# Kernel optimization log

Hardware: AMD Instinct MI355X
Metric: run time of the kernel (lower is better)

The kernel has to match this reference:

```python
import jax, jax.numpy as jnp
import numpy as np

RES_DIM = 8192
BATCH = 128
DENSITY = 0.02
NNZ = int(DENSITY * RES_DIM * RES_DIM)  # 1342177
LEAK = 0.6
BIAS = 1.6


def setup_inputs() -> dict:
    key = jax.random.key(0)
    k1, k2, k3, k4, k5 = jax.random.split(key, 5)
    proj_vars = jax.random.normal(k1, (BATCH, RES_DIM), dtype=jnp.float32)
    res_state = jax.random.normal(k2, (BATCH, RES_DIM), dtype=jnp.float32)
    # COO representation of the sparse reservoir matrix wr (what BCOO stores).
    # Values scaled so the effective spectral radius is O(spec_rad), keeping
    # tanh out of full saturation (init-time normalization detail).
    scale = 0.8 / np.sqrt(DENSITY * RES_DIM)
    wr_vals = jax.random.normal(k3, (NNZ,), dtype=jnp.float32) * scale
    wr_rows = jnp.sort(jax.random.randint(k4, (NNZ,), 0, RES_DIM, dtype=jnp.int32))
    wr_cols = jax.random.randint(k5, (NNZ,), 0, RES_DIM, dtype=jnp.int32)
    return {
        "proj_vars": proj_vars,
        "res_state": res_state,
        "wr_vals": wr_vals,
        "wr_rows": wr_rows,
        "wr_cols": wr_cols,
    }


def reference(proj_vars, res_state, wr_vals, wr_rows, wr_cols):
    # Batched sparse matvec: y[b, i] = sum_k vals[k] * res_state[b, cols[k]] for rows[k]==i
    # gather -> [nnz, batch], scale by vals, scatter-add over rows (sorted).
    contrib = wr_vals[:, None] * res_state.T[wr_cols]           # [nnz, B]
    y = jax.ops.segment_sum(contrib, wr_rows, num_segments=RES_DIM,
                            indices_are_sorted=True)            # [res_dim, B]
    res_next = jnp.tanh(y.T + proj_vars + BIAS)                  # [B, res_dim]
    return LEAK * res_next + (1.0 - LEAK) * res_state
```

## Files before the change

kernel.cpp:

```cpp
#include <hip/hip_runtime.h>
#include <hip/hip_bf16.h>
#include <stdint.h>

#define RES_DIM 8192
#define BATCH   128
#define NNZ     1342177
#define LEAK    0.6f
#define BIAS    1.6f

#define CONV_BLOCKS 1024
#define BND_BLOCKS  ((NNZ + 255) / 256)

__device__ __forceinline__ float fast_tanh(float x) {
    float e = __expf(2.0f * x);
    return 1.0f - 2.0f / (e + 1.0f);
}

__device__ __forceinline__ uint32_t f32_to_bf16_rne(float f) {
    uint32_t u = __float_as_uint(f);
    return (u + 0x7fffu + ((u >> 16) & 1u)) >> 16;
}

__global__ __launch_bounds__(256) void prep_kernel(
    const float* __restrict__ in, uint32_t* __restrict__ st2,
    const int* __restrict__ rows, int* __restrict__ row_start) {
    if (blockIdx.x < CONV_BLOCKS) {
        __shared__ float tile[32][33];
        const int bx = blockIdx.x & 255;
        const int by = blockIdx.x >> 8;
        const int tx = threadIdx.x & 31, ty = threadIdx.x >> 5;
        const int r0 = bx * 32, b0 = by * 32;
#pragma unroll
        for (int j = 0; j < 32; j += 8)
            tile[ty + j][tx] = in[(size_t)(b0 + ty + j) * RES_DIM + r0 + tx];
        __syncthreads();
        const int t = threadIdx.x;
#pragma unroll
        for (int i = t; i < 512; i += 256) {
            int rl = i >> 4, pl = i & 15;
            uint32_t lo = f32_to_bf16_rne(tile[2 * pl + 0][rl]);
            uint32_t hi = f32_to_bf16_rne(tile[2 * pl + 1][rl]);
            st2[(size_t)(r0 + rl) * 64 + (b0 >> 1) + pl] = lo | (hi << 16);
        }
    } else {
        const int k = (blockIdx.x - CONV_BLOCKS) * 256 + threadIdx.x;
        if (k >= NNZ) return;
        const int r1 = rows[k];
        if (k == 0)
            for (int r = 0; r <= r1; ++r) row_start[r] = 0;
        if (k + 1 < NNZ) {
            const int r2 = rows[k + 1];
            for (int r = r1 + 1; r <= r2; ++r) row_start[r] = k + 1;
        } else {
            for (int r = r1 + 1; r <= RES_DIM; ++r) row_start[r] = NNZ;
        }
    }
}

#define FMA8(G, v)                                            \
    do {                                                      \
        a0 = fmaf(v, __uint_as_float((G).x << 16), a0);       \
        a1 = fmaf(v, __uint_as_float((G).x & 0xffff0000u), a1); \
        a2 = fmaf(v, __uint_as_float((G).y << 16), a2);       \
        a3 = fmaf(v, __uint_as_float((G).y & 0xffff0000u), a3); \
        a4 = fmaf(v, __uint_as_float((G).z << 16), a4);       \
        a5 = fmaf(v, __uint_as_float((G).z & 0xffff0000u), a5); \
        a6 = fmaf(v, __uint_as_float((G).w << 16), a6);       \
        a7 = fmaf(v, __uint_as_float((G).w & 0xffff0000u), a7); \
    } while (0)

template <int BF16Y>
__global__ __launch_bounds__(256, 8) void spmm_kernel(
    const float* __restrict__ vals, const int* __restrict__ cols,
    const int* __restrict__ row_start, const uint32_t* __restrict__ st2,
    void* __restrict__ yT) {
    const int l = threadIdx.x & 63;
    const int g = l >> 4;
    const int j = l & 15;
    const int r = blockIdx.x * 4 + (threadIdx.x >> 6);

    const int ks = row_start[r];
    const int ke = row_start[r + 1];

    float a0 = 0, a1 = 0, a2 = 0, a3 = 0, a4 = 0, a5 = 0, a6 = 0, a7 = 0;
    const uint32_t* tp = st2 + j * 4;

    int k = ks;
    for (; k + 16 <= ke; k += 16) {
        const int k0 = k + g, k1 = k + 4 + g, k2 = k + 8 + g, k3 = k + 12 + g;
        const int c0 = cols[k0], c1 = cols[k1], c2 = cols[k2], c3 = cols[k3];
        const float v0 = vals[k0], v1 = vals[k1], v2 = vals[k2], v3 = vals[k3];
        const uint4 G0 = *(const uint4*)(tp + (size_t)c0 * 64);
        const uint4 G1 = *(const uint4*)(tp + (size_t)c1 * 64);
        const uint4 G2 = *(const uint4*)(tp + (size_t)c2 * 64);
        const uint4 G3 = *(const uint4*)(tp + (size_t)c3 * 64);
        FMA8(G0, v0);
        FMA8(G1, v1);
        FMA8(G2, v2);
        FMA8(G3, v3);
    }
    if (k < ke) {
#pragma unroll
        for (int i = 0; i < 4; ++i) {
            const int kk = k + 4 * i + g;
            int c = 0;
            float v = 0.0f;
            if (kk < ke) { c = cols[kk]; v = vals[kk]; }
            const uint4 G = *(const uint4*)(tp + (size_t)c * 64);
            FMA8(G, v);
        }
    }

    a0 += __shfl_xor(a0, 16, 64); a0 += __shfl_xor(a0, 32, 64);
    a1 += __shfl_xor(a1, 16, 64); a1 += __shfl_xor(a1, 32, 64);
    a2 += __shfl_xor(a2, 16, 64); a2 += __shfl_xor(a2, 32, 64);
    a3 += __shfl_xor(a3, 16, 64); a3 += __shfl_xor(a3, 32, 64);
    a4 += __shfl_xor(a4, 16, 64); a4 += __shfl_xor(a4, 32, 64);
    a5 += __shfl_xor(a5, 16, 64); a5 += __shfl_xor(a5, 32, 64);
    a6 += __shfl_xor(a6, 16, 64); a6 += __shfl_xor(a6, 32, 64);
    a7 += __shfl_xor(a7, 16, 64); a7 += __shfl_xor(a7, 32, 64);

    if (l < 16) {
        if (BF16Y) {
            uint32_t* o = (uint32_t*)yT + (size_t)r * 64 + j * 4;
            o[0] = f32_to_bf16_rne(a0) | (f32_to_bf16_rne(a1) << 16);
            o[1] = f32_to_bf16_rne(a2) | (f32_to_bf16_rne(a3) << 16);
            o[2] = f32_to_bf16_rne(a4) | (f32_to_bf16_rne(a5) << 16);
            o[3] = f32_to_bf16_rne(a6) | (f32_to_bf16_rne(a7) << 16);
        } else {
            float* o = (float*)yT + (size_t)r * BATCH + j * 8;
            *(float4*)(o + 0) = make_float4(a0, a1, a2, a3);
            *(float4*)(o + 4) = make_float4(a4, a5, a6, a7);
        }
    }
}

template <int BF16Y>
__global__ __launch_bounds__(256) void epi_kernel(
    const void* __restrict__ yT, const float* __restrict__ proj,
    const float* __restrict__ res, float* __restrict__ out) {
    __shared__ float tile[32][33];
    const int r0 = blockIdx.x * 32;
    const int b0 = blockIdx.y * 32;
    const int tx = threadIdx.x, ty = threadIdx.y;
#pragma unroll
    for (int jj = 0; jj < 32; jj += 8) {
        size_t idx = (size_t)(r0 + ty + jj) * BATCH + b0 + tx;
        float v;
        if (BF16Y) {
            uint32_t u = ((const uint16_t*)yT)[idx];
            v = __uint_as_float(u << 16);
        } else {
            v = ((const float*)yT)[idx];
        }
        tile[ty + jj][tx] = v;
    }
    __syncthreads();
#pragma unroll
    for (int jj = 0; jj < 32; jj += 8) {
        size_t oi = (size_t)(b0 + ty + jj) * RES_DIM + r0 + tx;
        float y = tile[tx][ty + jj] + proj[oi] + BIAS;
        out[oi] = LEAK * fast_tanh(y) + (1.0f - LEAK) * res[oi];
    }
}

extern "C" void kernel_launch(void* const* d_in, const int* in_sizes, int n_in,
                              void* d_out, int out_size, void* d_ws, size_t ws_size,
                              hipStream_t stream) {
    const float* proj      = (const float*)d_in[0];
    const float* res_state = (const float*)d_in[1];
    const float* wr_vals   = (const float*)d_in[2];
    const int*   wr_rows   = (const int*)d_in[3];
    const int*   wr_cols   = (const int*)d_in[4];
    float*       out       = (float*)d_out;

    uint8_t*  ws        = (uint8_t*)d_ws;
    uint32_t* st2       = (uint32_t*)ws;
    int*      row_start = (int*)(ws + 2097152);
    uint8_t*  yT        = ws + 2130176;
    const bool f32y = ws_size >= (2130176ull + (size_t)RES_DIM * BATCH * 4);

    prep_kernel<<<CONV_BLOCKS + BND_BLOCKS, 256, 0, stream>>>(
        res_state, st2, wr_rows, row_start);

    if (f32y) {
        spmm_kernel<0><<<RES_DIM / 4, 256, 0, stream>>>(wr_vals, wr_cols, row_start, st2, yT);
        epi_kernel<0><<<dim3(RES_DIM / 32, BATCH / 32), dim3(32, 8), 0, stream>>>(yT, proj, res_state, out);
    } else {
        spmm_kernel<1><<<RES_DIM / 4, 256, 0, stream>>>(wr_vals, wr_cols, row_start, st2, yT);
        epi_kernel<1><<<dim3(RES_DIM / 32, BATCH / 32), dim3(32, 8), 0, stream>>>(yT, proj, res_state, out);
    }
}
```

Before: 36.46 us.

## Split each SpMM row across four waves with vectorized index loads and LDS reduction

The SpMM kernel now assigns one row per block. The block's four waves split the row's nonzeros, and the kernel uses aligned int4/float4 loads of cols and vals, handles head and tail peeling in separate waves, and reduces partial sums through shared memory. Rows are also remapped across blocks with a strided index. The row-boundary builder processes four nonzeros per thread with vector loads, and the epilogue uses float4 loads and stores over 64-row tiles. This is meant to increase parallelism and memory-level concurrency per row, at the cost of an extra block-level barrier and reduction and four times as many blocks.

Result: no change. 35.79 us (-1.8%).

```diff
diff --git a/kernel.cpp b/kernel.cpp
--- a/kernel.cpp
+++ b/kernel.cpp
@@ -9,7 +9,8 @@
 #define BIAS    1.6f
 
 #define CONV_BLOCKS 1024
-#define BND_BLOCKS  ((NNZ + 255) / 256)
+#define BND_THREADS ((NNZ + 3) / 4)
+#define BND_BLOCKS  ((BND_THREADS + 255) / 256)
 
 __device__ __forceinline__ float fast_tanh(float x) {
     float e = __expf(2.0f * x);
@@ -34,38 +35,42 @@
         for (int j = 0; j < 32; j += 8)
             tile[ty + j][tx] = in[(size_t)(b0 + ty + j) * RES_DIM + r0 + tx];
         __syncthreads();
-        const int t = threadIdx.x;
-#pragma unroll
-        for (int i = t; i < 512; i += 256) {
+#pragma unroll
+        for (int i = threadIdx.x; i < 512; i += 256) {
             int rl = i >> 4, pl = i & 15;
             uint32_t lo = f32_to_bf16_rne(tile[2 * pl + 0][rl]);
             uint32_t hi = f32_to_bf16_rne(tile[2 * pl + 1][rl]);
             st2[(size_t)(r0 + rl) * 64 + (b0 >> 1) + pl] = lo | (hi << 16);
         }
     } else {
-        const int k = (blockIdx.x - CONV_BLOCKS) * 256 + threadIdx.x;
-        if (k >= NNZ) return;
-        const int r1 = rows[k];
-        if (k == 0)
-            for (int r = 0; r <= r1; ++r) row_start[r] = 0;
-        if (k + 1 < NNZ) {
-            const int r2 = rows[k + 1];
-            for (int r = r1 + 1; r <= r2; ++r) row_start[r] = k + 1;
+        const int t  = (blockIdx.x - CONV_BLOCKS) * 256 + threadIdx.x;
+        const int k4 = t * 4;
+        if (k4 >= NNZ) return;
+        if (k4 + 4 <= NNZ) {
+            const int4 R = *(const int4*)(rows + k4);
+            if (k4 == 0)
+                for (int r = 0; r <= R.x; ++r) row_start[r] = 0;
+            const int rn = rows[k4 + 4];
+            for (int r = R.x + 1; r <= R.y; ++r) row_start[r] = k4 + 1;
+            for (int r = R.y + 1; r <= R.z; ++r) row_start[r] = k4 + 2;
+            for (int r = R.z + 1; r <= R.w; ++r) row_start[r] = k4 + 3;
+            for (int r = R.w + 1; r <= rn;  ++r) row_start[r] = k4 + 4;
         } else {
+            const int r1 = rows[k4];
             for (int r = r1 + 1; r <= RES_DIM; ++r) row_start[r] = NNZ;
         }
     }
 }
 
-#define FMA8(G, v)                                            \
-    do {                                                      \
-        a0 = fmaf(v, __uint_as_float((G).x << 16), a0);       \
+#define FMA8(G, v)                                              \
+    do {                                                        \
+        a0 = fmaf(v, __uint_as_float((G).x << 16), a0);         \
         a1 = fmaf(v, __uint_as_float((G).x & 0xffff0000u), a1); \
-        a2 = fmaf(v, __uint_as_float((G).y << 16), a2);       \
+        a2 = fmaf(v, __uint_as_float((G).y << 16), a2);         \
         a3 = fmaf(v, __uint_as_float((G).y & 0xffff0000u), a3); \
-        a4 = fmaf(v, __uint_as_float((G).z << 16), a4);       \
+        a4 = fmaf(v, __uint_as_float((G).z << 16), a4);         \
         a5 = fmaf(v, __uint_as_float((G).z & 0xffff0000u), a5); \
-        a6 = fmaf(v, __uint_as_float((G).w << 16), a6);       \
+        a6 = fmaf(v, __uint_as_float((G).w << 16), a6);         \
         a7 = fmaf(v, __uint_as_float((G).w & 0xffff0000u), a7); \
     } while (0)
 
@@ -74,41 +79,51 @@
     const float* __restrict__ vals, const int* __restrict__ cols,
     const int* __restrict__ row_start, const uint32_t* __restrict__ st2,
     void* __restrict__ yT) {
-    const int l = threadIdx.x & 63;
+    const int t = threadIdx.x;
+    const int w = t >> 6;
+    const int l = t & 63;
     const int g = l >> 4;
     const int j = l & 15;
-    const int r = blockIdx.x * 4 + (threadIdx.x >> 6);
+    const int r = (blockIdx.x & 7) * (RES_DIM / 8) + (blockIdx.x >> 3);
 
     const int ks = row_start[r];
     const int ke = row_start[r + 1];
-
+    const int ka = min(ke, (ks + 3) & ~3);
+    const int U  = (ke - ka) >> 4;
+    const int ts = ka + (U << 4);
+
+    const uint32_t* tp = st2 + j * 4;
     float a0 = 0, a1 = 0, a2 = 0, a3 = 0, a4 = 0, a5 = 0, a6 = 0, a7 = 0;
-    const uint32_t* tp = st2 + j * 4;
-
-    int k = ks;
-    for (; k + 16 <= ke; k += 16) {
-        const int k0 = k + g, k1 = k + 4 + g, k2 = k + 8 + g, k3 = k + 12 + g;
-        const int c0 = cols[k0], c1 = cols[k1], c2 = cols[k2], c3 = cols[k3];
-        const float v0 = vals[k0], v1 = vals[k1], v2 = vals[k2], v3 = vals[k3];
-        const uint4 G0 = *(const uint4*)(tp + (size_t)c0 * 64);
-        const uint4 G1 = *(const uint4*)(tp + (size_t)c1 * 64);
-        const uint4 G2 = *(const uint4*)(tp + (size_t)c2 * 64);
-        const uint4 G3 = *(const uint4*)(tp + (size_t)c3 * 64);
-        FMA8(G0, v0);
-        FMA8(G1, v1);
-        FMA8(G2, v2);
-        FMA8(G3, v3);
-    }
-    if (k < ke) {
+
+    if (w == 0 && ks < ka) {
+        const int kk = ks + g;
+        int c = 0; float v = 0.0f;
+        if (kk < ka) { c = cols[kk]; v = vals[kk]; }
+        const uint4 G = *(const uint4*)(tp + (size_t)c * 64);
+        FMA8(G, v);
+    }
+    if (w == 1 && ts < ke) {
 #pragma unroll
         for (int i = 0; i < 4; ++i) {
-            const int kk = k + 4 * i + g;
-            int c = 0;
-            float v = 0.0f;
+            const int kk = ts + 4 * i + g;
+            int c = 0; float v = 0.0f;
             if (kk < ke) { c = cols[kk]; v = vals[kk]; }
             const uint4 G = *(const uint4*)(tp + (size_t)c * 64);
             FMA8(G, v);
         }
+    }
+    for (int u = w; u < U; u += 4) {
+        const int base = ka + (u << 4) + 4 * g;
+        const int4   C = *(const int4*)(cols + base);
+        const float4 V = *(const float4*)(vals + base);
+        const uint4 G0 = *(const uint4*)(tp + (size_t)C.x * 64);
+        const uint4 G1 = *(const uint4*)(tp + (size_t)C.y * 64);
+        const uint4 G2 = *(const uint4*)(tp + (size_t)C.z * 64);
+        const uint4 G3 = *(const uint4*)(tp + (size_t)C.w * 64);
+        FMA8(G0, V.x);
+        FMA8(G1, V.y);
+        FMA8(G2, V.z);
+        FMA8(G3, V.w);
     }
 
     a0 += __shfl_xor(a0, 16, 64); a0 += __shfl_xor(a0, 32, 64);
@@ -120,17 +135,22 @@
     a6 += __shfl_xor(a6, 16, 64); a6 += __shfl_xor(a6, 32, 64);
     a7 += __shfl_xor(a7, 16, 64); a7 += __shfl_xor(a7, 32, 64);
 
+    __shared__ float red[4][16][8];
     if (l < 16) {
+        *(float4*)&red[w][j][0] = make_float4(a0, a1, a2, a3);
+        *(float4*)&red[w][j][4] = make_float4(a4, a5, a6, a7);
+    }
+    __syncthreads();
+    if (t < BATCH) {
+        const int jj = t >> 3, ii = t & 7;
+        float s = red[0][jj][ii] + red[1][jj][ii] + red[2][jj][ii] + red[3][jj][ii];
         if (BF16Y) {
-            uint32_t* o = (uint32_t*)yT + (size_t)r * 64 + j * 4;
-            o[0] = f32_to_bf16_rne(a0) | (f32_to_bf16_rne(a1) << 16);
-            o[1] = f32_to_bf16_rne(a2) | (f32_to_bf16_rne(a3) << 16);
-            o[2] = f32_to_bf16_rne(a4) | (f32_to_bf16_rne(a5) << 16);
-            o[3] = f32_to_bf16_rne(a6) | (f32_to_bf16_rne(a7) << 16);
+            float shi = __shfl_down(s, 1, 64);
+            if (!(t & 1))
+                ((uint32_t*)yT)[(size_t)r * 64 + (t >> 1)] =
+                    f32_to_bf16_rne(s) | (f32_to_bf16_rne(shi) << 16);
         } else {
-            float* o = (float*)yT + (size_t)r * BATCH + j * 8;
-            *(float4*)(o + 0) = make_float4(a0, a1, a2, a3);
-            *(float4*)(o + 4) = make_float4(a4, a5, a6, a7);
+            ((float*)yT)[(size_t)r * BATCH + t] = s;
         }
     }
 }
@@ -139,28 +159,44 @@
 __global__ __launch_bounds__(256) void epi_kernel(
     const void* __restrict__ yT, const float* __restrict__ proj,
     const float* __restrict__ res, float* __restrict__ out) {
-    __shared__ float tile[32][33];
-    const int r0 = blockIdx.x * 32;
+    __shared__ float tile[64][33];
+    const int r0 = blockIdx.x * 64;
     const int b0 = blockIdx.y * 32;
-    const int tx = threadIdx.x, ty = threadIdx.y;
-#pragma unroll
-    for (int jj = 0; jj < 32; jj += 8) {
-        size_t idx = (size_t)(r0 + ty + jj) * BATCH + b0 + tx;
-        float v;
+    const int t  = threadIdx.x;
+#pragma unroll
+    for (int p = 0; p < 2; ++p) {
+        const int rl = p * 32 + (t >> 3);
+        const int bq = (t & 7) * 4;
+        float x, y, z, wv;
         if (BF16Y) {
-            uint32_t u = ((const uint16_t*)yT)[idx];
-            v = __uint_as_float(u << 16);
+            ushort4 u = *(const ushort4*)((const uint16_t*)yT +
+                         (size_t)(r0 + rl) * BATCH + b0 + bq);
+            x  = __uint_as_float((uint32_t)u.x << 16);
+            y  = __uint_as_float((uint32_t)u.y << 16);
+            z  = __uint_as_float((uint32_t)u.z << 16);
+            wv = __uint_as_float((uint32_t)u.w << 16);
         } else {
-            v = ((const float*)yT)[idx];
-        }
-        tile[ty + jj][tx] = v;
+            float4 v = *(const float4*)((const float*)yT +
+                         (size_t)(r0 + rl) * BATCH + b0 + bq);
+            x = v.x; y = v.y; z = v.z; wv = v.w;
+        }
+        tile[rl][bq + 0] = x; tile[rl][bq + 1] = y;
+        tile[rl][bq + 2] = z; tile[rl][bq + 3] = wv;
     }
     __syncthreads();
 #pragma unroll
-    for (int jj = 0; jj < 32; jj += 8) {
-        size_t oi = (size_t)(b0 + ty + jj) * RES_DIM + r0 + tx;
-        float y = tile[tx][ty + jj] + proj[oi] + BIAS;
-        out[oi] = LEAK * fast_tanh(y) + (1.0f - LEAK) * res[oi];
+    for (int p = 0; p < 2; ++p) {
+        const int bl = p * 16 + (t >> 4);
+        const int rq = (t & 15) * 4;
+        const size_t oi = (size_t)(b0 + bl) * RES_DIM + r0 + rq;
+        const float4 pj = *(const float4*)(proj + oi);
+        const float4 rs = *(const float4*)(res + oi);
+        float4 o;
+        o.x = LEAK * fast_tanh(tile[rq + 0][bl] + pj.x + BIAS) + (1.0f - LEAK) * rs.x;
+        o.y = LEAK * fast_tanh(tile[rq + 1][bl] + pj.y + BIAS) + (1.0f - LEAK) * rs.y;
+        o.z = LEAK * fast_tanh(tile[rq + 2][bl] + pj.z + BIAS) + (1.0f - LEAK) * rs.z;
+        o.w = LEAK * fast_tanh(tile[rq + 3][bl] + pj.w + BIAS) + (1.0f - LEAK) * rs.w;
+        *(float4*)(out + oi) = o;
     }
 }
 
@@ -184,10 +220,10 @@
         res_state, st2, wr_rows, row_start);
 
     if (f32y) {
-        spmm_kernel<0><<<RES_DIM / 4, 256, 0, stream>>>(wr_vals, wr_cols, row_start, st2, yT);
-        epi_kernel<0><<<dim3(RES_DIM / 32, BATCH / 32), dim3(32, 8), 0, stream>>>(yT, proj, res_state, out);
+        spmm_kernel<0><<<RES_DIM, 256, 0, stream>>>(wr_vals, wr_cols, row_start, st2, yT);
+        epi_kernel<0><<<dim3(RES_DIM / 64, BATCH / 32), 256, 0, stream>>>(yT, proj, res_state, out);
     } else {
-        spmm_kernel<1><<<RES_DIM / 4, 256, 0, stream>>>(wr_vals, wr_cols, row_start, st2, yT);
-        epi_kernel<1><<<dim3(RES_DIM / 32, BATCH / 32), dim3(32, 8), 0, stream>>>(yT, proj, res_state, out);
-    }
-}
+        spmm_kernel<1><<<RES_DIM, 256, 0, stream>>>(wr_vals, wr_cols, row_start, st2, yT);
+        epi_kernel<1><<<dim3(RES_DIM / 64, BATCH / 32), 256, 0, stream>>>(yT, proj, res_state, out);
+    }
+}
```
